# Kernel tuning notes

Measured on AMD Instinct MI355X. Metric: run time of the kernel, lower is better.

## Reference

```python
import jax, jax.numpy as jnp
from jax import lax
import numpy as np

T, B, C, H, L, K = 512, 32, 512, 512, 2, 2  # time, batch, in_feat, hidden, layers, kernel


def setup_inputs() -> dict:
    key = jax.random.key(0)
    k0, k1, k2 = jax.random.split(key, 3)
    x = jax.random.normal(k0, (T, B, C), dtype=jnp.float32)
    # per layer: [n_dir=2, n_gate=4 (z,f,o,i), H, Cin, K] conv weights and [2,4,H] biases
    w0 = jax.random.normal(k1, (2, 4, H, C, K), dtype=jnp.float32) * 0.05
    b0 = jnp.zeros((2, 4, H), dtype=jnp.float32)
    w1 = jax.random.normal(k2, (2, 4, H, 2 * H, K), dtype=jnp.float32) * 0.05
    b1 = jnp.zeros((2, 4, H), dtype=jnp.float32)
    return {"x": x, "w0": w0, "b0": b0, "w1": w1, "b1": b1}


def _conv(x, w, b):
    # x: [B, Cin, T], w: [H, Cin, K]; left-pad K-1 zeros == torch cat([zeros, x]) + VALID conv
    y = lax.conv_general_dilated(x, w, (1,), [(K - 1, 0)],
                                 dimension_numbers=("NCH", "OIH", "NCH"))
    return y + b[None, :, None]


def _qrnn_layer(x, W, b, reverse):
    # x: [B, Cin, T]; W: [4, H, Cin, K]; b: [4, H]
    if reverse:
        x = x[:, :, ::-1]  # note: original code does NOT flip the output back
    z = jnp.tanh(_conv(x, W[0], b[0]))
    f = jax.nn.sigmoid(_conv(x, W[1], b[1]))  # eval-mode zoneout: 1-(1-sigmoid)=sigmoid
    o = jax.nn.sigmoid(_conv(x, W[2], b[2]))
    i = jax.nn.sigmoid(_conv(x, W[3], b[3]))
    iz = i * z
    f_t = jnp.moveaxis(f, 2, 0)   # [T, B, H]
    iz_t = jnp.moveaxis(iz, 2, 0)

    def step(c, fi):
        ft, izt = fi
        c = ft * c + izt  # IFO pooling recurrence
        return c, c

    _, cs = lax.scan(step, jnp.zeros(f_t.shape[1:], f.dtype), (f_t, iz_t))
    c = jnp.moveaxis(cs, 0, 2)  # [B, H, T]
    return o * c


def _forward(x, w0, b0, w1, b1):
    h = jnp.transpose(x, (1, 2, 0))  # [T,B,C] -> [B,C,T]
    h_lasts = []
    for W, bb in ((w0, b0), (w1, b1)):
        d0 = _qrnn_layer(h, W[0], bb[0], False)
        d1 = _qrnn_layer(h, W[1], bb[1], True)
        t_last = h.shape[2] - 2  # lengths.fill_(T-1); t_last = lengths - 1 = T-2 (faithful)
        h_lasts.append(jnp.concatenate([d0[:, :, t_last], d1[:, :, 0]], axis=1))  # [B, 2H]
        h = jnp.concatenate([d0, d1], axis=1)  # [B, 2H, T]
    output = jnp.transpose(h, (2, 0, 1))  # [T, B, 2H]
    h_n = jnp.stack(h_lasts, axis=0)      # [L, B, 2H]
    return output, h_n


def reference(x, w0, b0, w1, b1):
    return _forward(x, w0, b0, w1, b1)
```

## Files before the change

kernel.cpp:

```cpp
#include <hip/hip_runtime.h>
#include <cstddef>
#include <cstdint>

#define Tn 512
#define Bn 32
#define Hn 512
static const size_t PLANE = 8388608;

typedef float f32x4 __attribute__((ext_vector_type(4)));
typedef __bf16 bf16x8 __attribute__((ext_vector_type(8)));
typedef _Float16 h2 __attribute__((ext_vector_type(2)));

__device__ __forceinline__ float sigm(float x) { return 1.0f / (1.0f + __expf(-x)); }
__device__ __forceinline__ float tanh_fast(float x) { return 2.0f / (1.0f + __expf(-2.0f * x)) - 1.0f; }
__device__ __forceinline__ unsigned short f2bf(float f) {
    unsigned int u = __float_as_uint(f);
    u += 0x7FFF + ((u >> 16) & 1);
    return (unsigned short)(u >> 16);
}


__global__ __launch_bounds__(256) void conv_x(const float* __restrict__ x,
                                              unsigned short* __restrict__ xbf) {
    const int i = blockIdx.x * 256 + threadIdx.x;
    const int c8 = i & 63;
    const int tp = (i >> 6) % 514;
    const int b  = (i >> 6) / 514;
    unsigned short v[8];
    if (tp == 0 || tp == 513) {
#pragma unroll
        for (int j = 0; j < 8; ++j) v[j] = 0;
    } else {
        const float* s = x + ((size_t)(tp - 1) * Bn + b) * 512 + c8 * 8;
#pragma unroll
        for (int j = 0; j < 8; ++j) v[j] = f2bf(s[j]);
    }
    unsigned short* d = xbf + ((size_t)b * 514 + tp) * 512 + c8 * 8;
    *(uint4*)d = *(const uint4*)v;
}

__global__ __launch_bounds__(256) void conv_w2(const float* __restrict__ w0,
                                               const float* __restrict__ w1,
                                               unsigned short* __restrict__ w0bf,
                                               unsigned short* __restrict__ w1bf) {
    int i = blockIdx.x * 256 + threadIdx.x;
    const float* src;
    unsigned short* dst;
    int Cin;
    if (i < 4194304) { src = w0; dst = w0bf; Cin = 512; }
    else { i -= 4194304; src = w1; dst = w1bf; Cin = 1024; }
    const int K = 2 * Cin;
    const int dm2 = i / K;
    const int kp = i - dm2 * K;
    const int dir = dm2 >> 11;
    const int mp = dm2 & 2047;
    const int o = mp >> 2;
    const int g = mp & 3;
    const int tap = (kp >= Cin) ? 1 : 0;
    const int c = kp - tap * Cin;
    dst[i] = f2bf(src[((((size_t)dir * 4 + g) * 512 + o) * Cin + c) * 2 + tap]);
}

__global__ __launch_bounds__(256) void zero_h1pad(unsigned short* __restrict__ h1bf) {
    const int i = blockIdx.x * 256 + threadIdx.x;
    const int c = i & 1023;
    const int b = (i >> 10) & 31;
    const int tp = (i >> 15) ? 513 : 0;
    h1bf[((size_t)b * 514 + tp) * 1024 + c] = 0;
}

template <int CIN>
__global__ __launch_bounds__(256) void gate_gemm_bf16(
    const unsigned short* __restrict__ Wbf,
    const unsigned short* __restrict__ Xbf,
    const float* __restrict__ bias,
    h2* __restrict__ fiz,
    _Float16* __restrict__ osb,
    float* __restrict__ Fsum,
    float* __restrict__ Ssum)
{
    __shared__ __align__(16) unsigned char smem[32768];
    unsigned short* As = (unsigned short*)smem;
    unsigned short* Bs = (unsigned short*)(smem + 16384);

    const int tid = threadIdx.x;
    const int lane = tid & 63;
    const int wave = tid >> 6;
    const int n0 = blockIdx.x * 128;
    const int dir = blockIdx.y >> 4;
    const int m0 = (blockIdx.y & 15) * 128;
    const int wm = (wave & 1) * 64;
    const int wn = (wave >> 1) * 64;

    const unsigned short* Wb = Wbf + (size_t)dir * 2048 * 2 * CIN;

    const unsigned short* pA[4];
    const unsigned short* pB0[4];
    unsigned short* ldst[8];
#pragma unroll
    for (int r = 0; r < 4; ++r) {
        const int q = r * 256 + tid;
        const int row = q >> 3;
        const int j = q & 7;
        const int kk = j ^ ((row >> 1) & 7);
        pA[r] = Wb + (size_t)(m0 + row) * (2 * CIN) + kk * 8;
        const int n = n0 + row;
        const int t = n & 511;
        const int b = n >> 9;
        const int tp0 = dir ? (513 - t) : t;
        pB0[r] = Xbf + ((size_t)b * 514 + tp0) * CIN + kk * 8;
        ldst[r] = As + (size_t)q * 8;
        ldst[r + 4] = Bs + (size_t)q * 8;
    }
    const int dstep = dir ? -CIN : CIN;

    int offA[2][4], offB[2][4];
#pragma unroll
    for (int kh = 0; kh < 2; ++kh) {
        const int jr = (lane >> 4) + kh * 4;
#pragma unroll
        for (int f = 0; f < 4; ++f) {
            const int ma = wm + f * 16 + (lane & 15);
            offA[kh][f] = ma * 64 + (jr ^ ((ma >> 1) & 7)) * 8;
            const int nb = wn + f * 16 + (lane & 15);
            offB[kh][f] = nb * 64 + (jr ^ ((nb >> 1) & 7)) * 8;
        }
    }

    f32x4 acc[4][4] = {};

    auto mfma_stage = [&]() {
#pragma unroll
        for (int kh = 0; kh < 2; ++kh) {
            bf16x8 af[4], bfr[4];
#pragma unroll
            for (int f = 0; f < 4; ++f) {
                af[f] = *(const bf16x8*)&As[offA[kh][f]];
                bfr[f] = *(const bf16x8*)&Bs[offB[kh][f]];
            }
#pragma unroll
            for (int fm = 0; fm < 4; ++fm)
#pragma unroll
                for (int fn = 0; fn < 4; ++fn)
                    acc[fm][fn] = __builtin_amdgcn_mfma_f32_16x16x32_bf16(
                        af[fm], bfr[fn], acc[fm][fn], 0, 0, 0);
        }
    };

#define GL(P, D) __builtin_amdgcn_global_load_lds( \
        (const __attribute__((address_space(1))) unsigned int*)(P), \
        (__attribute__((address_space(3))) unsigned int*)(D), 16, 0, 0)

#pragma unroll
    for (int tap = 0; tap < 2; ++tap) {
        const unsigned short* a0 = pA[0] + tap * CIN;
        const unsigned short* a1 = pA[1] + tap * CIN;
        const unsigned short* a2 = pA[2] + tap * CIN;
        const unsigned short* a3 = pA[3] + tap * CIN;
        const unsigned short* b0 = pB0[0] + tap * dstep;
        const unsigned short* b1 = pB0[1] + tap * dstep;
        const unsigned short* b2 = pB0[2] + tap * dstep;
        const unsigned short* b3 = pB0[3] + tap * dstep;
#pragma unroll
        for (int s = 0; s < CIN / 64; ++s) {
            GL(a0, ldst[0]); GL(a1, ldst[1]);
            GL(a2, ldst[2]); GL(a3, ldst[3]);
            GL(b0, ldst[4]); GL(b1, ldst[5]);
            GL(b2, ldst[6]); GL(b3, ldst[7]);
            __builtin_amdgcn_s_waitcnt(0);
            __syncthreads();
            mfma_stage();
            __syncthreads();
            a0 += 64; a1 += 64; a2 += 64; a3 += 64;
            b0 += 64; b1 += 64; b2 += 64; b3 += 64;
        }
    }
#undef GL

    const int q = lane >> 4;
    const int o0 = (blockIdx.y & 15) * 32;
    const float* bb = bias + dir * 2048;
    float Bz[4], Bf[4], Bo[4], Bi[4];
#pragma unroll
    for (int fm = 0; fm < 4; ++fm) {
        const int o = o0 + (wm >> 2) + fm * 4 + q;
        Bz[fm] = bb[o];
        Bf[fm] = bb[512 + o];
        Bo[fm] = bb[1024 + o];
        Bi[fm] = bb[1536 + o];
    }
    h2* Lfiz = (h2*)smem;
    _Float16* Los = (_Float16*)(smem + 18432);
#pragma unroll
    for (int fm = 0; fm < 4; ++fm) {
        const int ol = (wm >> 2) + fm * 4 + q;
#pragma unroll
        for (int fn = 0; fn < 4; ++fn) {
            f32x4 v = acc[fm][fn];
            const float f  = sigm(v.y + Bf[fm]);
            const float iz = sigm(v.w + Bi[fm]) * tanh_fast(v.x + Bz[fm]);
            const float os = sigm(v.z + Bo[fm]);
            const int nl = wn + fn * 16 + (lane & 15);
            h2 p; p.x = (_Float16)f; p.y = (_Float16)iz;
            Lfiz[nl * 36 + ol] = p;
            Los[nl * 40 + ol] = (_Float16)os;
        }
    }
    __syncthreads();
    h2* fz = fiz + (size_t)dir * PLANE;
    _Float16* ob = osb + (size_t)dir * PLANE;
#pragma unroll
    for (int l = 0; l < 4; ++l) {
        const int idx = l * 256 + tid;
        const int row = idx >> 3;
        const int col = idx & 7;
        uint4 v = *(const uint4*)((const unsigned char*)smem + row * 144 + col * 16);
        ((uint4*)(fz + (size_t)(n0 + row) * 512 + o0))[col] = v;
    }
#pragma unroll
    for (int l = 0; l < 2; ++l) {
        const int idx = l * 256 + tid;
        const int row = idx >> 2;
        const int col = idx & 3;
        uint4 v = *(const uint4*)((const unsigned char*)smem + 18432 + row * 80 + col * 16);
        ((uint4*)(ob + (size_t)(n0 + row) * 512 + o0))[col] = v;
    }
    if (tid < 64) {
        const int ol = tid & 31;
        const int ch = tid >> 5;
        float F = 1.0f, S = 0.0f;
#pragma unroll
        for (int tt = 0; tt < 64; ++tt) {
            const h2 v = Lfiz[(ch * 64 + tt) * 36 + ol];
            const float f = (float)v.x;
            F *= f;
            S = f * S + (float)v.y;
        }
        const int b = n0 >> 9;
        const int chg = ((n0 & 511) >> 6) + ch;
        const int o = o0 + ol;
        const int sidx = dir * 131072 + chg * 16384 + b * 512 + o;
        Fsum[sidx] = F;
        Ssum[sidx] = S;
    }
}


__global__ __launch_bounds__(256) void scan_B(
    const float* __restrict__ Fsum, const float* __restrict__ Ssum,
    float* __restrict__ cstart)
{
    const int i = blockIdx.x * 256 + threadIdx.x;
    const int base = (i >> 14) * 131072 + (i & 16383);
    float c = 0.0f;
    for (int ch = 0; ch < 8; ++ch) {
        cstart[base + ch * 16384] = c;
        c = Fsum[base + ch * 16384] * c + Ssum[base + ch * 16384];
    }
}

__global__ __launch_bounds__(256) void scan_C(
    const h2* __restrict__ fiz, const _Float16* __restrict__ osb,
    const float* __restrict__ cstart, float* __restrict__ out,
    unsigned short* __restrict__ h1bf,
    float* __restrict__ hn, int isLayer2)
{
    const int idx = blockIdx.x * 256 + threadIdx.x;
    const int dir = idx >> 17;
    const int rem = idx & 131071;
    const int o = rem & 511;
    const int b = (rem >> 9) & 31;
    const int chunk = rem >> 14;
    const int dirH = dir * 512;
    float c = cstart[idx];
    const h2* fz = fiz + (size_t)dir * PLANE;
    const _Float16* ob = osb + (size_t)dir * PLANE;
    const int tbase = chunk * 64;
    for (int tt = 0; tt < 64; ++tt) {
        const int t = tbase + tt;
        const size_t idxg = ((size_t)(b * 512 + t)) * 512 + o;
        const h2 v = fz[idxg];
        const float f = (float)v.x;
        const float iz = (float)v.y;
        const float os = (float)ob[idxg];
        c = f * c + iz;
        const float outv = os * c;
        if (isLayer2) {
            out[((size_t)t * Bn + b) * 1024 + dirH + o] = outv;
        } else {
            h1bf[((size_t)b * 514 + (t + 1)) * 1024 + dirH + o] = f2bf(outv);
        }
        const bool isLast = (dir == 0) ? (t == Tn - 2) : (t == 0);
        if (isLast) hn[(size_t)b * 1024 + dirH + o] = outv;
    }
}

extern "C" void kernel_launch(void* const* d_in, const int* in_sizes, int n_in,
                              void* d_out, int out_size, void* d_ws, size_t ws_size,
                              hipStream_t stream) {
    const float* x  = (const float*)d_in[0];
    const float* w0 = (const float*)d_in[1];
    const float* b0 = (const float*)d_in[2];
    const float* w1 = (const float*)d_in[3];
    const float* b1 = (const float*)d_in[4];
    float* out = (float*)d_out;
    float* ws = (float*)d_ws;

    h2* fiz        = (h2*)ws;
    _Float16* osb  = (_Float16*)(ws + 16777216);
    float* Fsum    = ws + 16777216 + 8388608;
    float* Ssum    = Fsum + 262144;
    float* cst     = Ssum + 262144;
    unsigned short* xbf  = (unsigned short*)(cst + 262144);
    unsigned short* h1bf = xbf + (size_t)32 * 514 * 512;
    unsigned short* w0bf = h1bf + (size_t)32 * 514 * 1024;
    unsigned short* w1bf = w0bf + (size_t)2 * 2048 * 1024;
    float* hn = out + 16777216;

    conv_x<<<4112, 256, 0, stream>>>(x, xbf);
    conv_w2<<<49152, 256, 0, stream>>>(w0, w1, w0bf, w1bf);
    zero_h1pad<<<256, 256, 0, stream>>>(h1bf);

    const dim3 gg(128, 32);

    gate_gemm_bf16<512><<<gg, 256, 0, stream>>>(w0bf, xbf, b0, fiz, osb, Fsum, Ssum);
    scan_B<<<128, 256, 0, stream>>>(Fsum, Ssum, cst);
    scan_C<<<1024, 256, 0, stream>>>(fiz, osb, cst, out, h1bf, hn, 0);
    gate_gemm_bf16<1024><<<gg, 256, 0, stream>>>(w1bf, h1bf, b1, fiz, osb, Fsum, Ssum);
    scan_B<<<128, 256, 0, stream>>>(Fsum, Ssum, cst);
    scan_C<<<1024, 256, 0, stream>>>(fiz, osb, cst, out, h1bf, hn + 32768, 1);
}
```

Before: 654.7 us.

## Enlarge gate GEMM tiles to 256x256 with double-buffered LDS pipeline

The gate GEMM moves from 128x128 tiles with 256 threads to 256x256 tiles with 512 threads (8 waves, each computing 128x64). It uses 128 KB of LDS with double buffering, so the global-to-LDS loads for the next k-step are issued while the current step's MFMAs run. The k-loop is split into sub-phases with explicit barriers, lgkmcnt waits and s_setprio around the MFMA blocks. The aim is more data reuse per byte loaded and hidden load latency. The costs are fewer blocks (1024 instead of 4096), much higher register and LDS pressure that limits occupancy, and many more barriers per step.

```diff
diff --git a/kernel.cpp b/kernel.cpp
--- a/kernel.cpp
+++ b/kernel.cpp
@@ -70,7 +70,7 @@
 }
 
 template <int CIN>
-__global__ __launch_bounds__(256) void gate_gemm_bf16(
+__global__ __launch_bounds__(512, 2) void gate_gemm_bf16(
     const unsigned short* __restrict__ Wbf,
     const unsigned short* __restrict__ Xbf,
     const float* __restrict__ bias,
@@ -79,162 +79,192 @@
     float* __restrict__ Fsum,
     float* __restrict__ Ssum)
 {
-    __shared__ __align__(16) unsigned char smem[32768];
-    unsigned short* As = (unsigned short*)smem;
-    unsigned short* Bs = (unsigned short*)(smem + 16384);
+    __shared__ __align__(16) unsigned char smem[131072];
+    unsigned short* lds0 = (unsigned short*)smem;
 
     const int tid = threadIdx.x;
     const int lane = tid & 63;
     const int wave = tid >> 6;
-    const int n0 = blockIdx.x * 128;
-    const int dir = blockIdx.y >> 4;
-    const int m0 = (blockIdx.y & 15) * 128;
-    const int wm = (wave & 1) * 64;
-    const int wn = (wave >> 1) * 64;
+    const int wm = wave >> 2;
+    const int wn = wave & 3;
+    const int n0 = blockIdx.x * 256;
+    const int dir = blockIdx.y >> 3;
+    const int m0 = (blockIdx.y & 7) * 256;
+    const int S0 = CIN / 64;
+    const int NS = 2 * S0;
+    const int dstep = dir ? -CIN : CIN;
 
     const unsigned short* Wb = Wbf + (size_t)dir * 2048 * 2 * CIN;
 
-    const unsigned short* pA[4];
-    const unsigned short* pB0[4];
-    unsigned short* ldst[8];
+    const unsigned short* pAs[4];
+    const unsigned short* pBs[4];
 #pragma unroll
     for (int r = 0; r < 4; ++r) {
-        const int q = r * 256 + tid;
+        const int q = r * 512 + tid;
         const int row = q >> 3;
         const int j = q & 7;
         const int kk = j ^ ((row >> 1) & 7);
-        pA[r] = Wb + (size_t)(m0 + row) * (2 * CIN) + kk * 8;
+        pAs[r] = Wb + (size_t)(m0 + row) * (2 * CIN) + kk * 8;
         const int n = n0 + row;
         const int t = n & 511;
         const int b = n >> 9;
         const int tp0 = dir ? (513 - t) : t;
-        pB0[r] = Xbf + ((size_t)b * 514 + tp0) * CIN + kk * 8;
-        ldst[r] = As + (size_t)q * 8;
-        ldst[r + 4] = Bs + (size_t)q * 8;
-    }
-    const int dstep = dir ? -CIN : CIN;
-
-    int offA[2][4], offB[2][4];
-#pragma unroll
-    for (int kh = 0; kh < 2; ++kh) {
-        const int jr = (lane >> 4) + kh * 4;
-#pragma unroll
-        for (int f = 0; f < 4; ++f) {
-            const int ma = wm + f * 16 + (lane & 15);
-            offA[kh][f] = ma * 64 + (jr ^ ((ma >> 1) & 7)) * 8;
-            const int nb = wn + f * 16 + (lane & 15);
-            offB[kh][f] = nb * 64 + (jr ^ ((nb >> 1) & 7)) * 8;
-        }
-    }
-
-    f32x4 acc[4][4] = {};
-
-    auto mfma_stage = [&]() {
-#pragma unroll
-        for (int kh = 0; kh < 2; ++kh) {
-            bf16x8 af[4], bfr[4];
-#pragma unroll
-            for (int f = 0; f < 4; ++f) {
-                af[f] = *(const bf16x8*)&As[offA[kh][f]];
-                bfr[f] = *(const bf16x8*)&Bs[offB[kh][f]];
-            }
-#pragma unroll
-            for (int fm = 0; fm < 4; ++fm)
-#pragma unroll
-                for (int fn = 0; fn < 4; ++fn)
-                    acc[fm][fn] = __builtin_amdgcn_mfma_f32_16x16x32_bf16(
-                        af[fm], bfr[fn], acc[fm][fn], 0, 0, 0);
-        }
-    };
+        pBs[r] = Xbf + ((size_t)b * 514 + tp0) * CIN + kk * 8;
+    }
+
+    const int jr0 = lane >> 4;
+    int offA[8], offB[4];
+#pragma unroll
+    for (int f = 0; f < 8; ++f) {
+        const int ma = wm * 128 + f * 16 + (lane & 15);
+        offA[f] = ma * 64 + (jr0 ^ ((ma >> 1) & 7)) * 8;
+    }
+#pragma unroll
+    for (int f = 0; f < 4; ++f) {
+        const int nb = wn * 64 + f * 16 + (lane & 15);
+        offB[f] = nb * 64 + (jr0 ^ ((nb >> 1) & 7)) * 8;
+    }
+
+    f32x4 acc[8][4] = {};
 
 #define GL(P, D) __builtin_amdgcn_global_load_lds( \
         (const __attribute__((address_space(1))) unsigned int*)(P), \
         (__attribute__((address_space(3))) unsigned int*)(D), 16, 0, 0)
 
-#pragma unroll
-    for (int tap = 0; tap < 2; ++tap) {
-        const unsigned short* a0 = pA[0] + tap * CIN;
-        const unsigned short* a1 = pA[1] + tap * CIN;
-        const unsigned short* a2 = pA[2] + tap * CIN;
-        const unsigned short* a3 = pA[3] + tap * CIN;
-        const unsigned short* b0 = pB0[0] + tap * dstep;
-        const unsigned short* b1 = pB0[1] + tap * dstep;
-        const unsigned short* b2 = pB0[2] + tap * dstep;
-        const unsigned short* b3 = pB0[3] + tap * dstep;
-#pragma unroll
-        for (int s = 0; s < CIN / 64; ++s) {
-            GL(a0, ldst[0]); GL(a1, ldst[1]);
-            GL(a2, ldst[2]); GL(a3, ldst[3]);
-            GL(b0, ldst[4]); GL(b1, ldst[5]);
-            GL(b2, ldst[6]); GL(b3, ldst[7]);
-            __builtin_amdgcn_s_waitcnt(0);
-            __syncthreads();
-            mfma_stage();
-            __syncthreads();
-            a0 += 64; a1 += 64; a2 += 64; a3 += 64;
-            b0 += 64; b1 += 64; b2 += 64; b3 += 64;
-        }
+#define STAGE(ks, sel) do { \
+    const int tap_ = ((ks) >= S0) ? 1 : 0; \
+    const int aoff_ = tap_ * CIN + ((ks) - tap_ * S0) * 64; \
+    const int boff_ = tap_ * dstep + ((ks) - tap_ * S0) * 64; \
+    unsigned short* Ad_ = lds0 + (sel) * 32768 + tid * 8; \
+    unsigned short* Bd_ = Ad_ + 16384; \
+    GL(pAs[0] + aoff_, Ad_);          GL(pBs[0] + boff_, Bd_); \
+    GL(pAs[1] + aoff_, Ad_ + 4096);   GL(pBs[1] + boff_, Bd_ + 4096); \
+    GL(pAs[2] + aoff_, Ad_ + 8192);   GL(pBs[2] + boff_, Bd_ + 8192); \
+    GL(pAs[3] + aoff_, Ad_ + 12288);  GL(pBs[3] + boff_, Bd_ + 12288); \
+} while (0)
+
+#define RD_A(mh, kh) do { \
+    af[0] = *(const bf16x8*)&Ab[offA[(mh)*4+0] ^ ((kh)*32)]; \
+    af[1] = *(const bf16x8*)&Ab[offA[(mh)*4+1] ^ ((kh)*32)]; \
+    af[2] = *(const bf16x8*)&Ab[offA[(mh)*4+2] ^ ((kh)*32)]; \
+    af[3] = *(const bf16x8*)&Ab[offA[(mh)*4+3] ^ ((kh)*32)]; \
+} while (0)
+
+#define RD_B(kh) do { \
+    bfr[0] = *(const bf16x8*)&Bb[offB[0] ^ ((kh)*32)]; \
+    bfr[1] = *(const bf16x8*)&Bb[offB[1] ^ ((kh)*32)]; \
+    bfr[2] = *(const bf16x8*)&Bb[offB[2] ^ ((kh)*32)]; \
+    bfr[3] = *(const bf16x8*)&Bb[offB[3] ^ ((kh)*32)]; \
+} while (0)
+
+#define MM(mh) do { \
+    _Pragma("unroll") \
+    for (int f_ = 0; f_ < 4; ++f_) { \
+        _Pragma("unroll") \
+        for (int fn_ = 0; fn_ < 4; ++fn_) \
+            acc[(mh)*4+f_][fn_] = __builtin_amdgcn_mfma_f32_16x16x32_bf16( \
+                af[f_], bfr[fn_], acc[(mh)*4+f_][fn_], 0, 0, 0); \
+    } \
+} while (0)
+
+#define LGKM0 do { asm volatile("s_waitcnt lgkmcnt(0)" ::: "memory"); \
+                   __builtin_amdgcn_sched_barrier(0); } while (0)
+
+    STAGE(0, 0);
+    asm volatile("s_waitcnt vmcnt(0)" ::: "memory");
+    __builtin_amdgcn_s_barrier();
+
+#pragma unroll 2
+    for (int s = 0; s < NS; ++s) {
+        asm volatile("" ::: "memory");
+        const unsigned short* Ab = lds0 + (s & 1) * 32768;
+        const unsigned short* Bb = Ab + 16384;
+        bf16x8 af[4], bfr[4];
+        const bool pre = (s + 1 < NS);
+        if (pre) STAGE(s + 1, (s & 1) ^ 1);
+        RD_B(0); RD_A(0, 0);
+        __builtin_amdgcn_s_barrier();
+        LGKM0;
+        __builtin_amdgcn_s_setprio(1); MM(0); __builtin_amdgcn_s_setprio(0);
+        __builtin_amdgcn_s_barrier();
+        RD_A(1, 0);
+        __builtin_amdgcn_s_barrier();
+        LGKM0;
+        __builtin_amdgcn_s_setprio(1); MM(1); __builtin_amdgcn_s_setprio(0);
+        __builtin_amdgcn_s_barrier();
+        RD_B(1); RD_A(0, 1);
+        __builtin_amdgcn_s_barrier();
+        LGKM0;
+        __builtin_amdgcn_s_setprio(1); MM(0); __builtin_amdgcn_s_setprio(0);
+        __builtin_amdgcn_s_barrier();
+        RD_A(1, 1);
+        __builtin_amdgcn_s_barrier();
+        LGKM0;
+        __builtin_amdgcn_s_setprio(1); MM(1); __builtin_amdgcn_s_setprio(0);
+        if (pre) asm volatile("s_waitcnt vmcnt(0)" ::: "memory");
+        __builtin_amdgcn_s_barrier();
     }
 #undef GL
-
-    const int q = lane >> 4;
-    const int o0 = (blockIdx.y & 15) * 32;
+#undef STAGE
+#undef RD_A
+#undef RD_B
+#undef MM
+#undef LGKM0
+
+    const int q4 = lane >> 4;
+    const int o0 = (blockIdx.y & 7) * 64;
     const float* bb = bias + dir * 2048;
-    float Bz[4], Bf[4], Bo[4], Bi[4];
-#pragma unroll
-    for (int fm = 0; fm < 4; ++fm) {
-        const int o = o0 + (wm >> 2) + fm * 4 + q;
-        Bz[fm] = bb[o];
-        Bf[fm] = bb[512 + o];
-        Bo[fm] = bb[1024 + o];
-        Bi[fm] = bb[1536 + o];
-    }
     h2* Lfiz = (h2*)smem;
-    _Float16* Los = (_Float16*)(smem + 18432);
-#pragma unroll
-    for (int fm = 0; fm < 4; ++fm) {
-        const int ol = (wm >> 2) + fm * 4 + q;
+    _Float16* Los = (_Float16*)(smem + 69632);
+#pragma unroll
+    for (int fm = 0; fm < 8; ++fm) {
+        const int ol = wm * 32 + fm * 4 + q4;
+        const int o = o0 + ol;
+        const float Bz = bb[o];
+        const float Bf = bb[512 + o];
+        const float Bo = bb[1024 + o];
+        const float Bi = bb[1536 + o];
 #pragma unroll
         for (int fn = 0; fn < 4; ++fn) {
             f32x4 v = acc[fm][fn];
-            const float f  = sigm(v.y + Bf[fm]);
-            const float iz = sigm(v.w + Bi[fm]) * tanh_fast(v.x + Bz[fm]);
-            const float os = sigm(v.z + Bo[fm]);
-            const int nl = wn + fn * 16 + (lane & 15);
-            h2 p; p.x = (_Float16)f; p.y = (_Float16)iz;
-            Lfiz[nl * 36 + ol] = p;
-            Los[nl * 40 + ol] = (_Float16)os;
+            const float fg = sigm(v.y + Bf);
+            const float iz = sigm(v.w + Bi) * tanh_fast(v.x + Bz);
+            const float og = sigm(v.z + Bo);
+            const int nl = wn * 64 + fn * 16 + (lane & 15);
+            h2 p; p.x = (_Float16)fg; p.y = (_Float16)iz;
+            Lfiz[nl * 68 + ol] = p;
+            Los[nl * 72 + ol] = (_Float16)og;
         }
     }
     __syncthreads();
     h2* fz = fiz + (size_t)dir * PLANE;
     _Float16* ob = osb + (size_t)dir * PLANE;
 #pragma unroll
+    for (int l = 0; l < 8; ++l) {
+        const int idx = l * 512 + tid;
+        const int row = idx >> 4;
+        const int col = idx & 15;
+        uint4 v = *(const uint4*)((const unsigned char*)smem + row * 272 + col * 16);
+        ((uint4*)(fz + (size_t)(n0 + row) * 512 + o0))[col] = v;
+    }
+#pragma unroll
     for (int l = 0; l < 4; ++l) {
-        const int idx = l * 256 + tid;
+        const int idx = l * 512 + tid;
         const int row = idx >> 3;
         const int col = idx & 7;
-        uint4 v = *(const uint4*)((const unsigned char*)smem + row * 144 + col * 16);
-        ((uint4*)(fz + (size_t)(n0 + row) * 512 + o0))[col] = v;
-    }
-#pragma unroll
-    for (int l = 0; l < 2; ++l) {
-        const int idx = l * 256 + tid;
-        const int row = idx >> 2;
-        const int col = idx & 3;
-        uint4 v = *(const uint4*)((const unsigned char*)smem + 18432 + row * 80 + col * 16);
+        uint4 v = *(const uint4*)((const unsigned char*)smem + 69632 + row * 144 + col * 16);
         ((uint4*)(ob + (size_t)(n0 + row) * 512 + o0))[col] = v;
     }
-    if (tid < 64) {
-        const int ol = tid & 31;
-        const int ch = tid >> 5;
+    if (tid < 256) {
+        const int ol = tid & 63;
+        const int ch = tid >> 6;
         float F = 1.0f, S = 0.0f;
 #pragma unroll
         for (int tt = 0; tt < 64; ++tt) {
-            const h2 v = Lfiz[(ch * 64 + tt) * 36 + ol];
-            const float f = (float)v.x;
-            F *= f;
-            S = f * S + (float)v.y;
+            const h2 v = Lfiz[(ch * 64 + tt) * 68 + ol];
+            const float fv = (float)v.x;
+            F *= fv;
+            S = fv * S + (float)v.y;
         }
         const int b = n0 >> 9;
         const int chg = ((n0 & 511) >> 6) + ch;
@@ -321,12 +351,12 @@
     conv_w2<<<49152, 256, 0, stream>>>(w0, w1, w0bf, w1bf);
     zero_h1pad<<<256, 256, 0, stream>>>(h1bf);
 
-    const dim3 gg(128, 32);
-
-    gate_gemm_bf16<512><<<gg, 256, 0, stream>>>(w0bf, xbf, b0, fiz, osb, Fsum, Ssum);
+    const dim3 gg(64, 16);
+
+    gate_gemm_bf16<512><<<gg, 512, 0, stream>>>(w0bf, xbf, b0, fiz, osb, Fsum, Ssum);
     scan_B<<<128, 256, 0, stream>>>(Fsum, Ssum, cst);
     scan_C<<<1024, 256, 0, stream>>>(fiz, osb, cst, out, h1bf, hn, 0);
-    gate_gemm_bf16<1024><<<gg, 256, 0, stream>>>(w1bf, h1bf, b1, fiz, osb, Fsum, Ssum);
+    gate_gemm_bf16<1024><<<gg, 512, 0, stream>>>(w1bf, h1bf, b1, fiz, osb, Fsum, Ssum);
     scan_B<<<128, 256, 0, stream>>>(Fsum, Ssum, cst);
     scan_C<<<1024, 256, 0, stream>>>(fiz, osb, cst, out, h1bf, hn + 32768, 1);
 }
```

Measured after the change: 745.4 us. 13.9% more time.
